# Optimization experiments

Measured on AMD Instinct MI355X. Metric: run time of the kernel, lower is better.

## Reference

```python
import jax, jax.numpy as jnp
import numpy as np

N = 25600      # nodes
DEG = 16       # incoming edges per node
E = N * DEG    # 409600 edges
B = 8          # graphs in batch
F = 7          # node features
H = 300        # hidden_channels
L = 100        # latent_channels


def _mlp(h, W1, b1, W2, b2, W3, b3):
    h = jax.nn.relu(h @ W1 + b1)
    h = jax.nn.relu(h @ W2 + b2)
    return h @ W3 + b3


def _edge_layer(x, src, dst, params):
    # PyG MessagePassing(aggr='max'), flow source_to_target:
    # x_j = x[src] (edge_index[0]), x_i = x[dst] (edge_index[1])
    x_i = x[dst]
    x_j = x[src]
    m = _mlp(jnp.concatenate([x_i, x_j - x_i], axis=-1), *params)  # [E, out]
    # every node has >=1 incoming edge by construction, so no empty segments
    return jax.ops.segment_max(m, dst, num_segments=x.shape[0])


def setup_inputs() -> dict:
    key = jax.random.key(0)
    ks = jax.random.split(key, 24)
    x = jax.random.normal(ks[0], (N, F), jnp.float32)
    dst = jnp.repeat(jnp.arange(N, dtype=jnp.int32), DEG)          # every node covered
    src = jax.random.randint(ks[1], (E,), 0, N, dtype=jnp.int32)
    edge_index = jnp.stack([src, dst])                              # [2, E]
    batch = jnp.repeat(jnp.arange(B, dtype=jnp.int32), N // B)     # sorted graph ids

    def lin(k, i, o):
        return jax.random.normal(k, (i, o), jnp.float32) / jnp.sqrt(jnp.float32(i))

    def bias(k, o):
        return jax.random.normal(k, (o,), jnp.float32) * 0.01

    inp = dict(x=x, edge_index=edge_index, batch=batch)
    # layer 0 MLP: 2*F -> H -> H -> L
    inp.update(l0_W1=lin(ks[2], 2 * F, H), l0_b1=bias(ks[3], H),
               l0_W2=lin(ks[4], H, H),     l0_b2=bias(ks[5], H),
               l0_W3=lin(ks[6], H, L),     l0_b3=bias(ks[7], L))
    # layer 1 MLP: 2*L -> H -> H -> L
    inp.update(l1_W1=lin(ks[8], 2 * L, H), l1_b1=bias(ks[9], H),
               l1_W2=lin(ks[10], H, H),    l1_b2=bias(ks[11], H),
               l1_W3=lin(ks[12], H, L),    l1_b3=bias(ks[13], L))
    # final lin: 3*L -> L -> L -> 1
    inp.update(lin_W1=lin(ks[14], 3 * L, L), lin_b1=bias(ks[15], L),
               lin_W2=lin(ks[16], L, L),     lin_b2=bias(ks[17], L),
               lin_W3=lin(ks[18], L, 1),     lin_b3=bias(ks[19], 1))
    return inp


def reference(x, edge_index, batch,
              l0_W1, l0_b1, l0_W2, l0_b2, l0_W3, l0_b3,
              l1_W1, l1_b1, l1_W2, l1_b2, l1_W3, l1_b3,
              lin_W1, lin_b1, lin_W2, lin_b2, lin_W3, lin_b3):
    src, dst = edge_index[0], edge_index[1]
    h = _edge_layer(x, src, dst, (l0_W1, l0_b1, l0_W2, l0_b2, l0_W3, l0_b3))
    h = jax.nn.relu(h)
    h = _edge_layer(h, src, dst, (l1_W1, l1_b1, l1_W2, l1_b2, l1_W3, l1_b3))
    h = jax.nn.relu(h)                                              # [N, L]
    addp = jax.ops.segment_sum(h, batch, num_segments=B)
    cnt = jax.ops.segment_sum(jnp.ones((h.shape[0], 1), h.dtype), batch, num_segments=B)
    meanp = addp / cnt
    maxp = jax.ops.segment_max(h, batch, num_segments=B)
    pooled = jnp.concatenate([addp, meanp, maxp], axis=1)           # [B, 3L]
    return _mlp(pooled, lin_W1, lin_b1, lin_W2, lin_b2, lin_W3, lin_b3)  # [B, 1]
```

## Files before the change

kernel.cpp:

```cpp
#include <hip/hip_runtime.h>

#define NNODES 25600
#define DEG 16
#define BGRAPHS 8
#define NPG (NNODES / BGRAPHS)
#define FDIM 7
#define HDIM 300
#define LDIM 100
#define HP 320
#define UVW 640
#define NT1 20
#define KS1 10
#define NT2 7
#define KS2 10
#define H0W 128
#define SSTR 328

typedef __attribute__((ext_vector_type(8))) _Float16 half8;
typedef __attribute__((ext_vector_type(2))) _Float16 half2v;
typedef __attribute__((ext_vector_type(4))) float floatx4;

__device__ __forceinline__ unsigned short f2h(float f) {
    _Float16 h = (_Float16)f;
    return __builtin_bit_cast(unsigned short, h);
}

union UV4H { uint4 v; half2v h[4]; };

__device__ __forceinline__ unsigned short packB(const float* W, int Kreal, int Nreal,
                                                int KS, int rel)
{
    int j = rel & 7, lane = (rel >> 3) & 63, rem = rel >> 9;
    int ks = rem % KS, nt = rem / KS;
    int k = ks * 32 + ((lane >> 4) << 3) + j;
    int n = nt * 16 + (lane & 15);
    float v = (k < Kreal && n < Nreal) ? W[k * Nreal + n] : 0.f;
    return f2h(v);
}

__device__ __forceinline__ unsigned short packProjW(const float* W1, int Ksub,
                                                    int KS, int rel)
{
    int j = rel & 7, lane = (rel >> 3) & 63, rem = rel >> 9;
    int ks = rem % KS, nt = rem / KS;
    int k = ks * 32 + ((lane >> 4) << 3) + j;
    int n = nt * 16 + (lane & 15);
    float v = 0.f;
    if (k < Ksub) {
        if (n < HP) { if (n < HDIM) v = W1[k * HDIM + n] - W1[(k + Ksub) * HDIM + n]; }
        else { int m = n - HP; if (m < HDIM) v = W1[(k + Ksub) * HDIM + m]; }
    }
    return f2h(v);
}

#define S0 102400
#define S1 102400
#define S2 35840
#define S3 35840
#define S4 81920
#define S5 20480
#define S6 1920
#define PACK_TOTAL (S0+S1+S2+S3+S4+S5+S6)

__global__ __launch_bounds__(256) void pack_all_kernel(
    const float* __restrict__ l0_W1, const float* __restrict__ l0_b1,
    const float* __restrict__ l0_W2, const float* __restrict__ l0_b2,
    const float* __restrict__ l0_W3,
    const float* __restrict__ l1_W1, const float* __restrict__ l1_b1,
    const float* __restrict__ l1_W2, const float* __restrict__ l1_b2,
    const float* __restrict__ l1_W3,
    unsigned short* __restrict__ PB2_0, unsigned short* __restrict__ PB2_1,
    unsigned short* __restrict__ PB3_0, unsigned short* __restrict__ PB3_1,
    unsigned short* __restrict__ PW1,  unsigned short* __restrict__ PW0,
    float* __restrict__ b2p_0, float* __restrict__ b2p_1,
    float* __restrict__ bp1,   float* __restrict__ bp0)
{
    int idx = blockIdx.x * 256 + threadIdx.x;
    if (idx >= PACK_TOTAL) return;
    if (idx < S0) { PB2_0[idx] = packB(l0_W2, HDIM, HDIM, KS1, idx); return; }
    idx -= S0;
    if (idx < S1) { PB2_1[idx] = packB(l1_W2, HDIM, HDIM, KS1, idx); return; }
    idx -= S1;
    if (idx < S2) { PB3_0[idx] = packB(l0_W3, HDIM, LDIM, KS2, idx); return; }
    idx -= S2;
    if (idx < S3) { PB3_1[idx] = packB(l1_W3, HDIM, LDIM, KS2, idx); return; }
    idx -= S3;
    if (idx < S4) { PW1[idx] = packProjW(l1_W1, LDIM, 4, idx); return; }
    idx -= S4;
    if (idx < S5) { PW0[idx] = packProjW(l0_W1, FDIM, 1, idx); return; }
    idx -= S5;
    if (idx < 320)       { b2p_0[idx] = (idx < HDIM) ? l0_b2[idx] : 0.f; return; }
    if (idx < 640)       { int n = idx - 320; b2p_1[n] = (n < HDIM) ? l1_b2[n] : 0.f; return; }
    if (idx < 1280)      { int n = idx - 640; bp1[n] = (n < HDIM) ? l1_b1[n] : 0.f; return; }
    { int n = idx - 1280; bp0[n] = (n < HDIM) ? l0_b1[n] : 0.f; }
}

template<int KS, bool A_IS_X>
__global__ __launch_bounds__(256) void proj_gemm_kernel(
    const void* __restrict__ Asrc, const unsigned short* __restrict__ PW,
    const float* __restrict__ bp,
    unsigned short* __restrict__ UV)
{
    __shared__ unsigned short As[4 * KS * 64 * 8];
    __shared__ unsigned short S[64 * SSTR];
    const int t = threadIdx.x;
    const int row0 = blockIdx.x * 64;

    if constexpr (A_IS_X) {
        const float* x = (const float*)Asrc;
        int lane = t & 63, mt = t >> 6;
        int quad = lane >> 4;
        int grow = row0 + mt * 16 + (lane & 15);
        unsigned short oz[8];
#pragma unroll
        for (int j = 0; j < 8; ++j) {
            int k = quad * 8 + j;
            oz[j] = (k < FDIM) ? f2h(x[grow * FDIM + k]) : (unsigned short)0;
        }
        *(uint4*)(As + t * 8) = *(uint4*)oz;
    } else {
        const unsigned short* h = (const unsigned short*)Asrc;
#pragma unroll
        for (int i = 0; i < 4; ++i) {
            int s = t + 256 * i;
            int lane = s & 63;
            int ks = (s >> 6) % KS;
            int mt = s / (KS * 64);
            int grow = row0 + mt * 16 + (lane & 15);
            int k0 = ks * 32 + ((lane >> 4) << 3);
            *(uint4*)(As + s * 8) = *(const uint4*)(h + (size_t)grow * H0W + k0);
        }
    }
    __syncthreads();

    const int w = t >> 6, lane = t & 63, quad = lane >> 4, l15 = lane & 15;

    for (int g = 0; g < 2; ++g) {
        const int ntb = g * 20 + w * 5;
        floatx4 c[5][4];
#pragma unroll
        for (int i = 0; i < 5; ++i)
#pragma unroll
            for (int mt = 0; mt < 4; ++mt) c[i][mt] = (floatx4){0.f, 0.f, 0.f, 0.f};
#pragma unroll
        for (int ks = 0; ks < KS; ++ks) {
            half8 a[4];
#pragma unroll
            for (int mt = 0; mt < 4; ++mt)
                a[mt] = *(const half8*)(As + ((mt * KS + ks) * 64 + lane) * 8);
#pragma unroll
            for (int i = 0; i < 5; ++i) {
                half8 b = *(const half8*)(PW + (size_t)(((ntb + i) * KS + ks) * 64 + lane) * 8);
#pragma unroll
                for (int mt = 0; mt < 4; ++mt)
                    c[i][mt] = __builtin_amdgcn_mfma_f32_16x16x32_f16(a[mt], b, c[i][mt], 0, 0, 0);
            }
        }
        __syncthreads();
#pragma unroll
        for (int i = 0; i < 5; ++i) {
            int colp = (w * 5 + i) * 16 + l15;
            float bb = bp[g * 320 + colp];
#pragma unroll
            for (int mt = 0; mt < 4; ++mt) {
#pragma unroll
                for (int r = 0; r < 4; ++r) {
                    int row = mt * 16 + quad * 4 + r;
                    S[row * SSTR + colp] = f2h(c[i][mt][r] + bb);
                }
            }
        }
        __syncthreads();
#pragma unroll
        for (int it = 0; it < 10; ++it) {
            int s = t + 256 * it;
            int row = s / 40, c4 = s - row * 40;
            uint4 v = *(const uint4*)(S + row * SSTR + c4 * 8);
            *(uint4*)(UV + (size_t)(row0 + row) * UVW + g * 320 + c4 * 8) = v;
        }
    }
}

template<bool OUT_HALF>
__global__ __launch_bounds__(512, 4) void edge_mfma_kernel(
    const unsigned short* __restrict__ UV,
    const int* __restrict__ src,
    const unsigned short* __restrict__ PB2, const float* __restrict__ b2p,
    const unsigned short* __restrict__ PB3, const float* __restrict__ b3,
    void* __restrict__ hout)
{
    __shared__ unsigned short Zs[4 * KS1 * 64 * 8];

    const int t = threadIdx.x;
    const int node0 = blockIdx.x * 4;
    const int lane = t & 63;
    const int w = t >> 6;
    const int quad = lane >> 4;
    const int l15 = lane & 15;
    const int slane = lane ^ ((lane & 0x30) >> 3);

    const int row16 = lane >> 2;
    const int part  = lane & 3;
    const int fl    = row16 + 16 * part;
    const int phys  = fl ^ (part << 1);

    const half2v hzero = {(_Float16)0.f, (_Float16)0.f};

#pragma unroll
    for (int i = 0; i < 5; ++i) {
        int s = t + 512 * i;
        int ks = (s >> 6) % KS1;
        int mt = s / (KS1 * 64);
        int m = mt * 16 + row16;
        int k0 = ks * 32 + part * 8;
        int srcn = src[node0 * 16 + m];
        UV4H ud, vd, o;
        ud.v = *(const uint4*)(UV + (size_t)(node0 + mt) * UVW + k0);
        vd.v = *(const uint4*)(UV + (size_t)srcn * UVW + HP + k0);
#pragma unroll
        for (int d = 0; d < 4; ++d) {
            half2v s2 = ud.h[d] + vd.h[d];
            o.h[d] = __builtin_elementwise_max(s2, hzero);
        }
        *(uint4*)(Zs + ((mt * KS1 + ks) * 64 + phys) * 8) = o.v;
    }
    __syncthreads();

    const int cnt1  = (w < 4) ? 3 : 2;
    const int base1 = (w < 4) ? 3 * w : 12 + 2 * (w - 4);
    floatx4 c1[3][4];
#pragma unroll
    for (int i = 0; i < 3; ++i)
#pragma unroll
        for (int mt = 0; mt < 4; ++mt) c1[i][mt] = (floatx4){0.f, 0.f, 0.f, 0.f};
    for (int ks = 0; ks < KS1; ++ks) {
        half8 a[4];
#pragma unroll
        for (int mt = 0; mt < 4; ++mt)
            a[mt] = *(const half8*)(Zs + ((mt * KS1 + ks) * 64 + slane) * 8);
#pragma unroll
        for (int i = 0; i < 3; ++i) {
            if (i < cnt1) {
                half8 b = *(const half8*)(PB2 + (size_t)(((base1 + i) * KS1 + ks) * 64 + lane) * 8);
#pragma unroll
                for (int mt = 0; mt < 4; ++mt)
                    c1[i][mt] = __builtin_amdgcn_mfma_f32_16x16x32_f16(a[mt], b, c1[i][mt], 0, 0, 0);
            }
        }
    }
    __syncthreads();

#pragma unroll
    for (int i = 0; i < 3; ++i) {
        if (i < cnt1) {
            int col = (base1 + i) * 16 + l15;
            float b2v = b2p[col];
            int slotbase = (col >> 5) * 64 + (((col >> 3) & 3) << 4) + quad * 4;
            int j = col & 7;
#pragma unroll
            for (int mt = 0; mt < 4; ++mt) {
#pragma unroll
                for (int r = 0; r < 4; ++r) {
                    float v = fmaxf(c1[i][mt][r] + b2v, 0.f);
                    Zs[(mt * KS1 * 64 + slotbase + r) * 8 + j] = f2h(v);
                }
            }
        }
    }
    __syncthreads();

    floatx4 c2[4];
#pragma unroll
    for (int mt = 0; mt < 4; ++mt) c2[mt] = (floatx4){0.f, 0.f, 0.f, 0.f};
    if (w < NT2) {
        for (int ks = 0; ks < KS2; ++ks) {
            half8 a[4];
#pragma unroll
            for (int mt = 0; mt < 4; ++mt)
                a[mt] = *(const half8*)(Zs + ((mt * KS2 + ks) * 64 + lane) * 8);
            half8 b = *(const half8*)(PB3 + (size_t)((w * KS2 + ks) * 64 + lane) * 8);
#pragma unroll
            for (int mt = 0; mt < 4; ++mt)
                c2[mt] = __builtin_amdgcn_mfma_f32_16x16x32_f16(a[mt], b, c2[mt], 0, 0, 0);
        }
    }

#pragma unroll
    for (int mt = 0; mt < 4; ++mt) {
        int node = node0 + mt;
        if (w < NT2) {
            int col = w * 16 + l15;
            floatx4 a = c2[mt];
            float mx = fmaxf(fmaxf(a[0], a[1]), fmaxf(a[2], a[3]));
            mx = fmaxf(mx, __shfl_xor(mx, 16, 64));
            mx = fmaxf(mx, __shfl_xor(mx, 32, 64));
            if (quad == 0) {
                if (OUT_HALF) {
                    unsigned short val = 0;
                    if (col < LDIM) val = f2h(fmaxf(mx + b3[col], 0.f));
                    ((unsigned short*)hout)[(size_t)node * H0W + col] = val;
                } else {
                    if (col < LDIM)
                        ((float*)hout)[(size_t)node * LDIM + col] = fmaxf(mx + b3[col], 0.f);
                }
            }
        }
        if (OUT_HALF && w == 7 && quad == 0)
            ((unsigned short*)hout)[(size_t)node * H0W + 112 + l15] = 0;
    }
}

__global__ __launch_bounds__(128) void pool1_kernel(
    const float* __restrict__ h, float* __restrict__ part)
{
    int g = blockIdx.x / 25;
    int sl = blockIdx.x % 25;
    int t = threadIdx.x;
    int base = g * NPG + sl * 128;
    if (t < LDIM) {
        float s = 0.f, mx = -1e30f;
        for (int i = 0; i < 128; ++i) {
            float v = h[(size_t)(base + i) * LDIM + t];
            s += v;
            mx = fmaxf(mx, v);
        }
        part[(size_t)blockIdx.x * 200 + t] = s;
        part[(size_t)blockIdx.x * 200 + 100 + t] = mx;
    }
}

__global__ __launch_bounds__(256) void final_kernel(
    const float* __restrict__ part,
    const float* __restrict__ W1, const float* __restrict__ b1,
    const float* __restrict__ W2, const float* __restrict__ b2,
    const float* __restrict__ W3, const float* __restrict__ b3,
    float* __restrict__ out)
{
    __shared__ float P[BGRAPHS][3 * LDIM];
    __shared__ float T1[BGRAPHS][LDIM];
    __shared__ float T2[BGRAPHS][LDIM];
    int t = threadIdx.x;
    for (int i = t; i < BGRAPHS * LDIM; i += 256) {
        int g = i / LDIM, f = i - (i / LDIM) * LDIM;
        float s = 0.f, mx = -1e30f;
        for (int sl = 0; sl < 25; ++sl) {
            s += part[(size_t)(g * 25 + sl) * 200 + f];
            mx = fmaxf(mx, part[(size_t)(g * 25 + sl) * 200 + 100 + f]);
        }
        P[g][f] = s;
        P[g][LDIM + f] = s * (1.0f / NPG);
        P[g][2 * LDIM + f] = mx;
    }
    __syncthreads();
    for (int i = t; i < BGRAPHS * LDIM; i += 256) {
        int g = i / LDIM, c = i - (i / LDIM) * LDIM;
        float a = b1[c];
        for (int k = 0; k < 3 * LDIM; ++k) a = fmaf(P[g][k], W1[k * LDIM + c], a);
        T1[g][c] = fmaxf(a, 0.f);
    }
    __syncthreads();
    for (int i = t; i < BGRAPHS * LDIM; i += 256) {
        int g = i / LDIM, c = i - (i / LDIM) * LDIM;
        float a = b2[c];
        for (int k = 0; k < LDIM; ++k) a = fmaf(T1[g][k], W2[k * LDIM + c], a);
        T2[g][c] = fmaxf(a, 0.f);
    }
    __syncthreads();
    if (t < BGRAPHS) {
        float a = b3[0];
        for (int k = 0; k < LDIM; ++k) a = fmaf(T2[t][k], W3[k], a);
        out[t] = a;
    }
}

extern "C" void kernel_launch(void* const* d_in, const int* in_sizes, int n_in,
                              void* d_out, int out_size, void* d_ws, size_t ws_size,
                              hipStream_t stream)
{
    const float* x      = (const float*)d_in[0];
    const int*   src    = (const int*)d_in[1];
    const float* l0_W1  = (const float*)d_in[3];
    const float* l0_b1  = (const float*)d_in[4];
    const float* l0_W2  = (const float*)d_in[5];
    const float* l0_b2  = (const float*)d_in[6];
    const float* l0_W3  = (const float*)d_in[7];
    const float* l0_b3  = (const float*)d_in[8];
    const float* l1_W1  = (const float*)d_in[9];
    const float* l1_b1  = (const float*)d_in[10];
    const float* l1_W2  = (const float*)d_in[11];
    const float* l1_b2  = (const float*)d_in[12];
    const float* l1_W3  = (const float*)d_in[13];
    const float* l1_b3  = (const float*)d_in[14];
    const float* lin_W1 = (const float*)d_in[15];
    const float* lin_b1 = (const float*)d_in[16];
    const float* lin_W2 = (const float*)d_in[17];
    const float* lin_b2 = (const float*)d_in[18];
    const float* lin_W3 = (const float*)d_in[19];
    const float* lin_b3 = (const float*)d_in[20];
    float* out = (float*)d_out;

    char* p = (char*)d_ws;
    unsigned short* UV    = (unsigned short*)p;  p += (size_t)NNODES * UVW * 2;
    unsigned short* h0b   = (unsigned short*)p;  p += (size_t)NNODES * H0W * 2;
    float* h1             = (float*)p;           p += (size_t)NNODES * LDIM * 4;
    unsigned short* PB2_0 = (unsigned short*)p;  p += (size_t)S0 * 2;
    unsigned short* PB2_1 = (unsigned short*)p;  p += (size_t)S1 * 2;
    unsigned short* PB3_0 = (unsigned short*)p;  p += (size_t)S2 * 2;
    unsigned short* PB3_1 = (unsigned short*)p;  p += (size_t)S3 * 2;
    unsigned short* PW1   = (unsigned short*)p;  p += (size_t)S4 * 2;
    unsigned short* PW0   = (unsigned short*)p;  p += (size_t)S5 * 2;
    float* b2p_0          = (float*)p;           p += HP * 4;
    float* b2p_1          = (float*)p;           p += HP * 4;
    float* bp1            = (float*)p;           p += 640 * 4;
    float* bp0            = (float*)p;           p += 640 * 4;
    float* part           = (float*)p;           p += (size_t)200 * 200 * 4;

    pack_all_kernel<<<(PACK_TOTAL + 255) / 256, 256, 0, stream>>>(
        l0_W1, l0_b1, l0_W2, l0_b2, l0_W3,
        l1_W1, l1_b1, l1_W2, l1_b2, l1_W3,
        PB2_0, PB2_1, PB3_0, PB3_1, PW1, PW0, b2p_0, b2p_1, bp1, bp0);

    proj_gemm_kernel<1, true><<<NNODES / 64, 256, 0, stream>>>(x, PW0, bp0, UV);
    edge_mfma_kernel<true><<<NNODES / 4, 512, 0, stream>>>(UV, src, PB2_0, b2p_0, PB3_0, l0_b3, h0b);
    proj_gemm_kernel<4, false><<<NNODES / 64, 256, 0, stream>>>(h0b, PW1, bp1, UV);
    edge_mfma_kernel<false><<<NNODES / 4, 512, 0, stream>>>(UV, src, PB2_1, b2p_1, PB3_1, l1_b3, h1);
    pool1_kernel<<<200, 128, 0, stream>>>(h1, part);
    final_kernel<<<1, 256, 0, stream>>>(part, lin_W1, lin_b1, lin_W2, lin_b2, lin_W3, lin_b3, out);
}
```

Measured before the change: 439.4 us.

## Make edge kernel persistent with double-buffered async LDS gather of source rows

The edge MLP kernel becomes persistent: 512 blocks loop over 4-node groups instead of launching one block per group. Two LDS buffers are used, and the gathered source-node V rows for the next group are prefetched with global_load_lds while the current group's MFMA runs. The MFMA operand order is swapped so the epilogue can write packed 8-byte values, and s_setprio raises wave priority during the matrix loops. The aim is to hide gather latency and launch overhead, at the cost of doubled LDS and hand-managed waitcnt barriers that lower occupancy.

New measurement: 928.5 us. 2.11x slower.

```diff
diff --git a/kernel.cpp b/kernel.cpp
--- a/kernel.cpp
+++ b/kernel.cpp
@@ -15,6 +15,8 @@
 #define KS2 10
 #define H0W 128
 #define SSTR 328
+#define NBLK 512
+#define NGROUP (NNODES / 4)
 
 typedef __attribute__((ext_vector_type(8))) _Float16 half8;
 typedef __attribute__((ext_vector_type(2))) _Float16 half2v;
@@ -26,6 +28,17 @@
 }
 
 union UV4H { uint4 v; half2v h[4]; };
+
+__device__ __forceinline__ void load_lds16(const void* gsrc, void* ldst) {
+    __builtin_amdgcn_global_load_lds(
+        (const __attribute__((address_space(1))) void*)gsrc,
+        (__attribute__((address_space(3))) void*)ldst, 16, 0, 0);
+}
+
+#define BAR_LDS() do { \
+    asm volatile("s_waitcnt lgkmcnt(0)" ::: "memory"); \
+    __builtin_amdgcn_s_barrier(); \
+    asm volatile("" ::: "memory"); } while (0)
 
 __device__ __forceinline__ unsigned short packB(const float* W, int Kreal, int Nreal,
                                                 int KS, int rel)
@@ -189,124 +202,184 @@
     const unsigned short* __restrict__ PB3, const float* __restrict__ b3,
     void* __restrict__ hout)
 {
-    __shared__ unsigned short Zs[4 * KS1 * 64 * 8];
+    __shared__ unsigned short ZA[4 * KS1 * 64 * 8];
+    __shared__ unsigned short ZB[4 * KS1 * 64 * 8];
 
     const int t = threadIdx.x;
-    const int node0 = blockIdx.x * 4;
     const int lane = t & 63;
     const int w = t >> 6;
     const int quad = lane >> 4;
     const int l15 = lane & 15;
-    const int slane = lane ^ ((lane & 0x30) >> 3);
-
-    const int row16 = lane >> 2;
-    const int part  = lane & 3;
-    const int fl    = row16 + 16 * part;
-    const int phys  = fl ^ (part << 1);
-
     const half2v hzero = {(_Float16)0.f, (_Float16)0.f};
-
-#pragma unroll
-    for (int i = 0; i < 5; ++i) {
-        int s = t + 512 * i;
-        int ks = (s >> 6) % KS1;
-        int mt = s / (KS1 * 64);
-        int m = mt * 16 + row16;
-        int k0 = ks * 32 + part * 8;
-        int srcn = src[node0 * 16 + m];
-        UV4H ud, vd, o;
-        ud.v = *(const uint4*)(UV + (size_t)(node0 + mt) * UVW + k0);
-        vd.v = *(const uint4*)(UV + (size_t)srcn * UVW + HP + k0);
-#pragma unroll
-        for (int d = 0; d < 4; ++d) {
-            half2v s2 = ud.h[d] + vd.h[d];
-            o.h[d] = __builtin_elementwise_max(s2, hzero);
-        }
-        *(uint4*)(Zs + ((mt * KS1 + ks) * 64 + phys) * 8) = o.v;
-    }
-    __syncthreads();
 
     const int cnt1  = (w < 4) ? 3 : 2;
     const int base1 = (w < 4) ? 3 * w : 12 + 2 * (w - 4);
-    floatx4 c1[3][4];
-#pragma unroll
-    for (int i = 0; i < 3; ++i)
-#pragma unroll
-        for (int mt = 0; mt < 4; ++mt) c1[i][mt] = (floatx4){0.f, 0.f, 0.f, 0.f};
-    for (int ks = 0; ks < KS1; ++ks) {
-        half8 a[4];
-#pragma unroll
-        for (int mt = 0; mt < 4; ++mt)
-            a[mt] = *(const half8*)(Zs + ((mt * KS1 + ks) * 64 + slane) * 8);
+
+    const int g0 = blockIdx.x;
+
+    {
+        int sidx[5];
+#pragma unroll
+        for (int q = 0; q < 5; ++q) {
+            int ii = w + 8 * q;
+            sidx[q] = src[g0 * 64 + (ii / 10) * 16 + l15];
+        }
+#pragma unroll
+        for (int q = 0; q < 5; ++q) {
+            int ii = w + 8 * q;
+            const unsigned short* gp =
+                UV + (size_t)sidx[q] * UVW + HP + (ii % 10) * 32 + quad * 8;
+            load_lds16(gp, ZA + ii * 512);
+        }
+    }
+
+    auto process = [&](unsigned short* __restrict__ cur,
+                       unsigned short* __restrict__ nxt, int g) {
+        const int node0 = g * 4;
+        const int gn = g + NBLK;
+        const bool have_next = gn < NGROUP;
+
+        asm volatile("s_waitcnt vmcnt(0) lgkmcnt(0)" ::: "memory");
+        __builtin_amdgcn_s_barrier();
+        asm volatile("" ::: "memory");
+
+        uint4 ur[5];
+#pragma unroll
+        for (int i = 0; i < 5; ++i) {
+            int s = t + 512 * i;
+            int mt = s / 640;
+            int k0 = ((s >> 6) % 10) * 32 + ((s >> 4) & 3) * 8;
+            ur[i] = *(const uint4*)(UV + (size_t)(node0 + mt) * UVW + k0);
+        }
+        int sidx[5];
+        if (have_next) {
+#pragma unroll
+            for (int q = 0; q < 5; ++q) {
+                int ii = w + 8 * q;
+                sidx[q] = src[gn * 64 + (ii / 10) * 16 + l15];
+            }
+        }
+#pragma unroll
+        for (int i = 0; i < 5; ++i) {
+            int soff = (t + 512 * i) * 8;
+            UV4H uu, vv, o;
+            uu.v = ur[i];
+            vv.v = *(const uint4*)(cur + soff);
+#pragma unroll
+            for (int d = 0; d < 4; ++d)
+                o.h[d] = __builtin_elementwise_max(uu.h[d] + vv.h[d], hzero);
+            *(uint4*)(cur + soff) = o.v;
+        }
+
+        BAR_LDS();
+
+        floatx4 c1[3][4];
+#pragma unroll
+        for (int i = 0; i < 3; ++i)
+#pragma unroll
+            for (int mt = 0; mt < 4; ++mt) c1[i][mt] = (floatx4){0.f, 0.f, 0.f, 0.f};
+        __builtin_amdgcn_s_setprio(1);
+        for (int ks = 0; ks < KS1; ++ks) {
+            half8 zb[4];
+#pragma unroll
+            for (int mt = 0; mt < 4; ++mt)
+                zb[mt] = *(const half8*)(cur + ((mt * KS1 + ks) * 64 + lane) * 8);
+#pragma unroll
+            for (int i = 0; i < 3; ++i) {
+                if (i < cnt1) {
+                    half8 wa = *(const half8*)(PB2 + (size_t)(((base1 + i) * KS1 + ks) * 64 + lane) * 8);
+#pragma unroll
+                    for (int mt = 0; mt < 4; ++mt)
+                        c1[i][mt] = __builtin_amdgcn_mfma_f32_16x16x32_f16(wa, zb[mt], c1[i][mt], 0, 0, 0);
+                }
+            }
+        }
+        __builtin_amdgcn_s_setprio(0);
+
+        if (have_next) {
+#pragma unroll
+            for (int q = 0; q < 5; ++q) {
+                int ii = w + 8 * q;
+                const unsigned short* gp =
+                    UV + (size_t)sidx[q] * UVW + HP + (ii % 10) * 32 + quad * 8;
+                load_lds16(gp, nxt + ii * 512);
+            }
+        }
+
+        BAR_LDS();
+
 #pragma unroll
         for (int i = 0; i < 3; ++i) {
             if (i < cnt1) {
-                half8 b = *(const half8*)(PB2 + (size_t)(((base1 + i) * KS1 + ks) * 64 + lane) * 8);
+                int B = base1 + i;
+                floatx4 bb = *(const floatx4*)(b2p + B * 16 + quad * 4);
+                int ks = B >> 1;
+                int khi = (2 * B + (quad >> 1)) & 3;
+                int jo = (quad & 1) * 4;
+#pragma unroll
+                for (int mt = 0; mt < 4; ++mt) {
+                    union { unsigned short us[4]; unsigned long long ll; } o;
+#pragma unroll
+                    for (int r = 0; r < 4; ++r)
+                        o.us[r] = f2h(fmaxf(c1[i][mt][r] + bb[r], 0.f));
+                    *(unsigned long long*)(cur + ((mt * KS1 + ks) * 64 + l15 + 16 * khi) * 8 + jo) = o.ll;
+                }
+            }
+        }
+
+        BAR_LDS();
+
+        floatx4 c2[4];
+#pragma unroll
+        for (int mt = 0; mt < 4; ++mt) c2[mt] = (floatx4){0.f, 0.f, 0.f, 0.f};
+        if (w < NT2) {
+            __builtin_amdgcn_s_setprio(1);
+            for (int ks = 0; ks < KS2; ++ks) {
+                half8 a[4];
 #pragma unroll
                 for (int mt = 0; mt < 4; ++mt)
-                    c1[i][mt] = __builtin_amdgcn_mfma_f32_16x16x32_f16(a[mt], b, c1[i][mt], 0, 0, 0);
-            }
-        }
-    }
-    __syncthreads();
-
-#pragma unroll
-    for (int i = 0; i < 3; ++i) {
-        if (i < cnt1) {
-            int col = (base1 + i) * 16 + l15;
-            float b2v = b2p[col];
-            int slotbase = (col >> 5) * 64 + (((col >> 3) & 3) << 4) + quad * 4;
-            int j = col & 7;
-#pragma unroll
-            for (int mt = 0; mt < 4; ++mt) {
-#pragma unroll
-                for (int r = 0; r < 4; ++r) {
-                    float v = fmaxf(c1[i][mt][r] + b2v, 0.f);
-                    Zs[(mt * KS1 * 64 + slotbase + r) * 8 + j] = f2h(v);
+                    a[mt] = *(const half8*)(cur + ((mt * KS2 + ks) * 64 + lane) * 8);
+                half8 b = *(const half8*)(PB3 + (size_t)((w * KS2 + ks) * 64 + lane) * 8);
+#pragma unroll
+                for (int mt = 0; mt < 4; ++mt)
+                    c2[mt] = __builtin_amdgcn_mfma_f32_16x16x32_f16(a[mt], b, c2[mt], 0, 0, 0);
+            }
+            __builtin_amdgcn_s_setprio(0);
+        }
+
+#pragma unroll
+        for (int mt = 0; mt < 4; ++mt) {
+            int node = node0 + mt;
+            if (w < NT2) {
+                int col = w * 16 + l15;
+                floatx4 a = c2[mt];
+                float mx = fmaxf(fmaxf(a[0], a[1]), fmaxf(a[2], a[3]));
+                mx = fmaxf(mx, __shfl_xor(mx, 16, 64));
+                mx = fmaxf(mx, __shfl_xor(mx, 32, 64));
+                if (quad == 0) {
+                    if (OUT_HALF) {
+                        unsigned short val = 0;
+                        if (col < LDIM) val = f2h(fmaxf(mx + b3[col], 0.f));
+                        ((unsigned short*)hout)[(size_t)node * H0W + col] = val;
+                    } else {
+                        if (col < LDIM)
+                            ((float*)hout)[(size_t)node * LDIM + col] = fmaxf(mx + b3[col], 0.f);
+                    }
                 }
             }
-        }
-    }
-    __syncthreads();
-
-    floatx4 c2[4];
-#pragma unroll
-    for (int mt = 0; mt < 4; ++mt) c2[mt] = (floatx4){0.f, 0.f, 0.f, 0.f};
-    if (w < NT2) {
-        for (int ks = 0; ks < KS2; ++ks) {
-            half8 a[4];
-#pragma unroll
-            for (int mt = 0; mt < 4; ++mt)
-                a[mt] = *(const half8*)(Zs + ((mt * KS2 + ks) * 64 + lane) * 8);
-            half8 b = *(const half8*)(PB3 + (size_t)((w * KS2 + ks) * 64 + lane) * 8);
-#pragma unroll
-            for (int mt = 0; mt < 4; ++mt)
-                c2[mt] = __builtin_amdgcn_mfma_f32_16x16x32_f16(a[mt], b, c2[mt], 0, 0, 0);
-        }
-    }
-
-#pragma unroll
-    for (int mt = 0; mt < 4; ++mt) {
-        int node = node0 + mt;
-        if (w < NT2) {
-            int col = w * 16 + l15;
-            floatx4 a = c2[mt];
-            float mx = fmaxf(fmaxf(a[0], a[1]), fmaxf(a[2], a[3]));
-            mx = fmaxf(mx, __shfl_xor(mx, 16, 64));
-            mx = fmaxf(mx, __shfl_xor(mx, 32, 64));
-            if (quad == 0) {
-                if (OUT_HALF) {
-                    unsigned short val = 0;
-                    if (col < LDIM) val = f2h(fmaxf(mx + b3[col], 0.f));
-                    ((unsigned short*)hout)[(size_t)node * H0W + col] = val;
-                } else {
-                    if (col < LDIM)
-                        ((float*)hout)[(size_t)node * LDIM + col] = fmaxf(mx + b3[col], 0.f);
-                }
-            }
-        }
-        if (OUT_HALF && w == 7 && quad == 0)
-            ((unsigned short*)hout)[(size_t)node * H0W + 112 + l15] = 0;
+            if (OUT_HALF && w == 7 && quad == 0)
+                ((unsigned short*)hout)[(size_t)node * H0W + 112 + l15] = 0;
+        }
+    };
+
+    int g = g0;
+    while (true) {
+        process(ZA, ZB, g);
+        g += NBLK;
+        if (g >= NGROUP) break;
+        process(ZB, ZA, g);
+        g += NBLK;
+        if (g >= NGROUP) break;
     }
 }
 
@@ -421,9 +494,9 @@
         PB2_0, PB2_1, PB3_0, PB3_1, PW1, PW0, b2p_0, b2p_1, bp1, bp0);
 
     proj_gemm_kernel<1, true><<<NNODES / 64, 256, 0, stream>>>(x, PW0, bp0, UV);
-    edge_mfma_kernel<true><<<NNODES / 4, 512, 0, stream>>>(UV, src, PB2_0, b2p_0, PB3_0, l0_b3, h0b);
+    edge_mfma_kernel<true><<<NBLK, 512, 0, stream>>>(UV, src, PB2_0, b2p_0, PB3_0, l0_b3, h0b);
     proj_gemm_kernel<4, false><<<NNODES / 64, 256, 0, stream>>>(h0b, PW1, bp1, UV);
-    edge_mfma_kernel<false><<<NNODES / 4, 512, 0, stream>>>(UV, src, PB2_1, b2p_1, PB3_1, l1_b3, h1);
+    edge_mfma_kernel<false><<<NBLK, 512, 0, stream>>>(UV, src, PB2_1, b2p_1, PB3_1, l1_b3, h1);
     pool1_kernel<<<200, 128, 0, stream>>>(h1, part);
     final_kernel<<<1, 256, 0, stream>>>(part, lin_W1, lin_b1, lin_W2, lin_b2, lin_W3, lin_b3, out);
 }
```
